# Kernel optimization log

Measured on AMD Instinct MI355X. Metric: run time of the kernel, lower is better.

## Reference

```python
import jax, jax.numpy as jnp
import numpy as np

B, C, H, W = 8, 4, 384, 384


def setup_inputs() -> dict:
    key = jax.random.key(0)
    k1, k2 = jax.random.split(key)
    outputs = jax.random.normal(k1, (B, C, H, W), dtype=jnp.float32)
    targets = jax.random.randint(k2, (B, H, W), 0, C)  # every class present w.h.p.
    return {"outputs": outputs, "targets": targets}


def _edt(is_zero):
    """Exact 2D Euclidean distance transform, batched.

    is_zero: bool [B,C,H,W], True at 'feature' pixels (distance 0 there).
    Returns float32 [B,C,H,W] distance to nearest True pixel.
    Separable exact algorithm (Meijster/Felzenszwalb-Huttenlocher style):
      phase 1: 1D distance along H via forward+backward scans;
      phase 2: dt^2(x,y) = min_j g(x,j)^2 + (y-j)^2 via a scan over y.
    """
    b, c, h, w = is_zero.shape
    BIG = jnp.float32(h + w)  # finite sentinel (exceeds any true distance)

    def pass1(carry, z):
        d = jnp.where(z, jnp.float32(0.0), jnp.minimum(carry + 1.0, BIG))
        return d, d

    init = jnp.full((b, c, w), BIG, jnp.float32)
    zt = jnp.moveaxis(is_zero, 2, 0)  # [H,B,C,W]
    _, fwd = jax.lax.scan(pass1, init, zt)
    _, bwd = jax.lax.scan(pass1, init, zt[::-1])
    g = jnp.minimum(fwd, bwd[::-1])          # [H,B,C,W] vertical 1D distances
    g2 = jnp.moveaxis(g * g, 0, 2)           # [B,C,H,W]

    j = jnp.arange(w, dtype=jnp.float32)     # candidate columns

    def pass2(_, y):
        # min over j of g(x,j)^2 + (y-j)^2  -> [B,C,H]
        return 0, jnp.min(g2 + (y - j) ** 2, axis=-1)

    _, dt2 = jax.lax.scan(pass2, 0, j)       # [W,B,C,H]
    return jnp.sqrt(jnp.moveaxis(dt2, 0, 3))  # [B,C,H,W]


def reference(outputs, targets):
    num_classes = outputs.shape[1]
    # one-hot: true_hot[b,c,h,w] = (targets[b,h,w] == c)
    true_hot = targets[:, None, :, :] == jnp.arange(num_classes)[None, :, None, None]
    dt = _edt(true_hot)                                  # 0 at class pixels
    dmax = jnp.max(dt, axis=(2, 3), keepdims=True)       # per (b,c) slice max
    dist_map = jnp.where(true_hot, -dmax, dt)            # factor = -1
    # weight=None -> ones(C); weight_matrix/weight.sum() == 1/C
    loss = jax.nn.softmax(outputs, axis=1) * dist_map / jnp.float32(num_classes)
    return jnp.mean(loss)
```

## Files before the change

### kernel.cpp

```cpp
#include <hip/hip_runtime.h>

#define B 8
#define C 4
#define H 384
#define W 384
#define HW (H * W)
#define CHW (C * H * W)
#define NTOT (B * CHW)
#define BIG2 589824
#define TPI 576
#define NBLK (B * TPI)
#define NSEG (B * H * 6)
#define LOG2E 1.44269504088896340736f

__device__ __forceinline__ int nearest2(unsigned long long m, int lx, int shl) {
    unsigned long long right = m >> lx;
    int dR = right ? (int)__builtin_ctzll(right) : 999;
    unsigned long long leftb = m << shl;
    int dL = leftb ? (int)__builtin_clzll(leftb) : 999;
    int d = min(dR, dL);
    return d * d;
}

__device__ __attribute__((noinline))
int ring_fallback(const int* __restrict__ tg, int xa, int ya, int c, int best) {
    for (int d = 17; d * d < best; ++d) {
        int xlo = xa - d, xhi = xa + d, ylo = ya - d, yhi = ya + d;
        for (int xx = max(xlo, 0); xx <= min(xhi, W - 1); ++xx) {
            int ddx = xx - xa;
            int bb = ddx * ddx + d * d;
            if (bb < best) {
                if (ylo >= 0 && tg[ylo * W + xx] == c) best = bb;
                if (yhi < H && tg[yhi * W + xx] == c) best = min(best, bb);
            }
        }
        for (int yy = max(ylo + 1, 0); yy <= min(yhi - 1, H - 1); ++yy) {
            int ddy = yy - ya;
            int bb = ddy * ddy + d * d;
            if (bb < best) {
                if (xlo >= 0 && tg[yy * W + xlo] == c) best = bb;
                if (xhi < W && tg[yy * W + xhi] == c) best = min(best, bb);
            }
        }
    }
    return best;
}

__global__ __launch_bounds__(256)
void build_masks(const int* __restrict__ targets,
                 unsigned long long* __restrict__ masks) {
    int wv = threadIdx.x >> 6, lane = threadIdx.x & 63;
    int seg = blockIdx.x * 4 + wv;
    if (seg >= NSEG) return;
    int wd = seg % 6, rem = seg / 6;
    int tv = targets[rem * W + wd * 64 + lane];
    unsigned long long m0 = __ballot(tv == 0);
    unsigned long long m1 = __ballot(tv == 1);
    unsigned long long m2 = __ballot(tv == 2);
    unsigned long long m3 = __ballot(tv == 3);
    if (lane == 0) {
        unsigned long long* dst = masks + (size_t)rem * 24 + wd;
        dst[0]  = m0;
        dst[6]  = m1;
        dst[12] = m2;
        dst[18] = m3;
    }
}

__global__ __launch_bounds__(256)
void dist_loss_kernel(const float* __restrict__ outputs,
                      const int* __restrict__ targets,
                      const unsigned long long* __restrict__ masks,
                      float* __restrict__ parts) {
    __shared__ unsigned long long rowsm[40][4];
    __shared__ unsigned long long big[8 * 18];
    __shared__ float sred[4][9];

    int bid = blockIdx.x;
    int bx = bid % 12, by = (bid / 12) % 48, b = bid / TPI;
    int x0 = bx * 32, y0 = by * 8;
    int tid = threadIdx.x, lane = tid & 63, wv = tid >> 6;
    const int* tg = targets + b * HW;

    if (tid < 160) {
        int r = tid >> 2, cc = tid & 3;
        int yaS = y0 - 16 + r;
        unsigned long long wmask = 0ull;
        if (yaS >= 0 && yaS < H) {
            const unsigned long long* mrow =
                masks + ((size_t)(b * H + yaS)) * 24 + cc * 6;
            int bitpos = x0 - 16;
            int iw = bitpos >> 6, sh = bitpos & 63;
            unsigned long long lo = (iw >= 0) ? mrow[iw] : 0ull;
            unsigned long long hi = (iw + 1 < 6) ? mrow[iw + 1] : 0ull;
            wmask = (lo >> sh) | (hi << (64 - sh));
        }
        rowsm[r][cc] = wmask;
    }
    __syncthreads();

    if (tid < 128) {
        int yy = tid >> 4, c = (tid >> 2) & 3, lvl = tid & 3;
        unsigned long long v = (lvl == 0)
            ? rowsm[16 + yy][c]
            : (rowsm[16 + yy - lvl][c] | rowsm[16 + yy + lvl][c]);
        big[yy * 18 + c * 4 + lvl] = v;
    }
    __syncthreads();

    int x = tid & 31, y = tid >> 5;
    int xa = x0 + x, ya = y0 + y, ly = y + 16;
    int lx = x + 16, shl = 63 - lx;

    float red[9];
    #pragma unroll
    for (int j = 0; j < 9; ++j) red[j] = 0.0f;

    const float* ob = outputs + (size_t)b * CHW + (size_t)ya * W + xa;
    float e0 = exp2f(ob[0] * LOG2E);
    float e1 = exp2f(ob[HW] * LOG2E);
    float e2 = exp2f(ob[2 * HW] * LOG2E);
    float e3 = exp2f(ob[3 * HW] * LOG2E);
    float inv = 1.0f / (e0 + e1 + e2 + e3);
    float pr[4] = {e0 * inv, e1 * inv, e2 * inv, e3 * inv};

    #pragma unroll
    for (int c = 0; c < 4; ++c) {
        const ulonglong2* pp = (const ulonglong2*)&big[y * 18 + c * 4];
        ulonglong2 v0 = pp[0], v1 = pp[1];
        int n0 = nearest2(v0.x, lx, shl);
        int n1 = nearest2(v0.y, lx, shl) + 1;
        int n2 = nearest2(v1.x, lx, shl) + 4;
        int n3 = nearest2(v1.y, lx, shl) + 9;
        int best = min(min(n0, n1), min(n2, n3));
        if (best > 16) {
            for (int dy = 4; dy <= 16 && dy * dy < best; ++dy) {
                unsigned long long m = rowsm[ly + dy][c] | rowsm[ly - dy][c];
                if (m) best = min(best, dy * dy + nearest2(m, lx, shl));
            }
            if (best > 289) {
                best = min(best, BIG2);
                best = ring_fallback(tg, xa, ya, c, best);
            }
        }
        float dt = sqrtf((float)best);
        red[0] += pr[c] * dt;
        if ((v0.x >> lx) & 1ull) red[1 + c] += pr[c];
        red[5 + c] = fmaxf(red[5 + c], dt);
    }

    #pragma unroll
    for (int off = 32; off > 0; off >>= 1) {
        #pragma unroll
        for (int j = 0; j < 5; ++j) red[j] += __shfl_down(red[j], off);
        #pragma unroll
        for (int j = 5; j < 9; ++j) red[j] = fmaxf(red[j], __shfl_down(red[j], off));
    }
    if (lane == 0) {
        #pragma unroll
        for (int j = 0; j < 9; ++j) sred[wv][j] = red[j];
    }
    __syncthreads();
    if (tid == 0) {
        float o[9];
        #pragma unroll
        for (int j = 0; j < 9; ++j) o[j] = sred[0][j];
        #pragma unroll
        for (int w = 1; w < 4; ++w) {
            #pragma unroll
            for (int j = 0; j < 5; ++j) o[j] += sred[w][j];
            #pragma unroll
            for (int j = 5; j < 9; ++j) o[j] = fmaxf(o[j], sred[w][j]);
        }
        #pragma unroll
        for (int j = 0; j < 9; ++j) parts[j * NBLK + bid] = o[j];
    }
}

__global__ __launch_bounds__(256)
void finalize(const float* __restrict__ parts, float* __restrict__ out) {
    __shared__ double asum[4];
    __shared__ double Tsh[32];
    __shared__ float Msh[32];
    int tid = threadIdx.x, lane = tid & 63, wv = tid >> 6;

    double a = 0.0;
    for (int i = tid; i < NBLK; i += 256) a += (double)parts[i];
    #pragma unroll
    for (int off = 32; off > 0; off >>= 1) a += __shfl_down(a, off);
    if (lane == 0) asum[wv] = a;

    for (int k = 0; k < 8; ++k) {
        int s = wv * 8 + k;
        int bb = s >> 2, cc = s & 3;
        double ts = 0.0;
        float ms = 0.0f;
        for (int i = lane; i < TPI; i += 64) {
            int blk = bb * TPI + i;
            ts += (double)parts[(1 + cc) * NBLK + blk];
            ms = fmaxf(ms, parts[(5 + cc) * NBLK + blk]);
        }
        #pragma unroll
        for (int off = 32; off > 0; off >>= 1) {
            ts += __shfl_down(ts, off);
            ms = fmaxf(ms, __shfl_down(ms, off));
        }
        if (lane == 0) { Tsh[s] = ts; Msh[s] = ms; }
    }
    __syncthreads();
    if (tid == 0) {
        double A = asum[0] + asum[1] + asum[2] + asum[3];
        double st = 0.0;
        for (int s = 0; s < 32; ++s) st += (double)Msh[s] * Tsh[s];
        out[0] = (float)((A - st) / ((double)C * (double)NTOT));
    }
}

extern "C" void kernel_launch(void* const* d_in, const int* in_sizes, int n_in,
                              void* d_out, int out_size, void* d_ws, size_t ws_size,
                              hipStream_t stream) {
    const float* outputs = (const float*)d_in[0];
    const int* targets = (const int*)d_in[1];
    float* out = (float*)d_out;
    float* parts = (float*)d_ws;
    unsigned long long* masks =
        (unsigned long long*)((char*)d_ws + 256 * 1024);

    build_masks<<<NSEG / 4, 256, 0, stream>>>(targets, masks);
    dist_loss_kernel<<<NBLK, 256, 0, stream>>>(outputs, targets, masks, parts);
    finalize<<<1, 256, 0, stream>>>(parts, out);
}
```

Baseline: 116.1 us.

## Fuse mask building into distance kernel with 64x8 tiles and 3-row halo

Removes the separate build_masks kernel: each block now ballots its own target bitmasks for a 14-row by 3-word halo into shared memory and runs the exact 3-row neighbourhood search directly on full 64-bit words. Tiles grow to 64x8 pixels with 512 threads, and the block reduction uses shuffles. The vertical halo drops from 16 rows to 3, so pixels whose best distance exceeds 16 now go straight to the scalar ring fallback starting at radius 4. This saves one launch and a global mask round trip, but the fallback may fire more often and targets get re-read redundantly across neighbouring blocks.

Result: no change. 115.7 us (-0.3%).

```diff
diff --git a/kernel.cpp b/kernel.cpp
--- a/kernel.cpp
+++ b/kernel.cpp
@@ -8,23 +8,13 @@
 #define CHW (C * H * W)
 #define NTOT (B * CHW)
 #define BIG2 589824
-#define TPI 576
+#define TPI 288
 #define NBLK (B * TPI)
-#define NSEG (B * H * 6)
 #define LOG2E 1.44269504088896340736f
-
-__device__ __forceinline__ int nearest2(unsigned long long m, int lx, int shl) {
-    unsigned long long right = m >> lx;
-    int dR = right ? (int)__builtin_ctzll(right) : 999;
-    unsigned long long leftb = m << shl;
-    int dL = leftb ? (int)__builtin_clzll(leftb) : 999;
-    int d = min(dR, dL);
-    return d * d;
-}
 
 __device__ __attribute__((noinline))
 int ring_fallback(const int* __restrict__ tg, int xa, int ya, int c, int best) {
-    for (int d = 17; d * d < best; ++d) {
+    for (int d = 4; d * d < best; ++d) {
         int xlo = xa - d, xhi = xa + d, ylo = ya - d, yhi = ya + d;
         for (int xx = max(xlo, 0); xx <= min(xhi, W - 1); ++xx) {
             int ddx = xx - xa;
@@ -46,106 +36,84 @@
     return best;
 }
 
-__global__ __launch_bounds__(256)
-void build_masks(const int* __restrict__ targets,
-                 unsigned long long* __restrict__ masks) {
-    int wv = threadIdx.x >> 6, lane = threadIdx.x & 63;
-    int seg = blockIdx.x * 4 + wv;
-    if (seg >= NSEG) return;
-    int wd = seg % 6, rem = seg / 6;
-    int tv = targets[rem * W + wd * 64 + lane];
-    unsigned long long m0 = __ballot(tv == 0);
-    unsigned long long m1 = __ballot(tv == 1);
-    unsigned long long m2 = __ballot(tv == 2);
-    unsigned long long m3 = __ballot(tv == 3);
-    if (lane == 0) {
-        unsigned long long* dst = masks + (size_t)rem * 24 + wd;
-        dst[0]  = m0;
-        dst[6]  = m1;
-        dst[12] = m2;
-        dst[18] = m3;
-    }
-}
-
-__global__ __launch_bounds__(256)
+__global__ __launch_bounds__(512)
 void dist_loss_kernel(const float* __restrict__ outputs,
                       const int* __restrict__ targets,
-                      const unsigned long long* __restrict__ masks,
                       float* __restrict__ parts) {
-    __shared__ unsigned long long rowsm[40][4];
-    __shared__ unsigned long long big[8 * 18];
-    __shared__ float sred[4][9];
+    __shared__ unsigned long long rowsm[14][3][4];
+    __shared__ float sred[8][9];
 
     int bid = blockIdx.x;
-    int bx = bid % 12, by = (bid / 12) % 48, b = bid / TPI;
-    int x0 = bx * 32, y0 = by * 8;
-    int tid = threadIdx.x, lane = tid & 63, wv = tid >> 6;
+    int b = bid / TPI;
+    int r = bid % TPI;
+    int wd = r / 48, yt = r % 48;
+    int tid = threadIdx.x, lane = tid & 63, wy = tid >> 6;
     const int* tg = targets + b * HW;
-
-    if (tid < 160) {
-        int r = tid >> 2, cc = tid & 3;
-        int yaS = y0 - 16 + r;
-        unsigned long long wmask = 0ull;
-        if (yaS >= 0 && yaS < H) {
-            const unsigned long long* mrow =
-                masks + ((size_t)(b * H + yaS)) * 24 + cc * 6;
-            int bitpos = x0 - 16;
-            int iw = bitpos >> 6, sh = bitpos & 63;
-            unsigned long long lo = (iw >= 0) ? mrow[iw] : 0ull;
-            unsigned long long hi = (iw + 1 < 6) ? mrow[iw + 1] : 0ull;
-            wmask = (lo >> sh) | (hi << (64 - sh));
-        }
-        rowsm[r][cc] = wmask;
+    int yr0 = yt * 8 - 3;
+
+    int xa = wd * 64 + lane;
+    int ya = yt * 8 + wy;
+
+    const float* ob = outputs + (size_t)b * CHW + (size_t)ya * W + xa;
+    float o0 = ob[0], o1 = ob[HW], o2 = ob[2 * HW], o3 = ob[3 * HW];
+
+    for (int t = wy; t < 42; t += 8) {
+        int rr = t / 3, wi = t % 3;
+        int yr = yr0 + rr, wg = wd - 1 + wi;
+        int tv = -1;
+        if (yr >= 0 && yr < H && wg >= 0 && wg < 6)
+            tv = tg[yr * W + wg * 64 + lane];
+        unsigned long long m0 = __ballot(tv == 0);
+        unsigned long long m1 = __ballot(tv == 1);
+        unsigned long long m2 = __ballot(tv == 2);
+        unsigned long long m3 = __ballot(tv == 3);
+        if (lane == 0) {
+            rowsm[rr][wi][0] = m0; rowsm[rr][wi][1] = m1;
+            rowsm[rr][wi][2] = m2; rowsm[rr][wi][3] = m3;
+        }
     }
     __syncthreads();
 
-    if (tid < 128) {
-        int yy = tid >> 4, c = (tid >> 2) & 3, lvl = tid & 3;
-        unsigned long long v = (lvl == 0)
-            ? rowsm[16 + yy][c]
-            : (rowsm[16 + yy - lvl][c] | rowsm[16 + yy + lvl][c]);
-        big[yy * 18 + c * 4 + lvl] = v;
-    }
-    __syncthreads();
-
-    int x = tid & 31, y = tid >> 5;
-    int xa = x0 + x, ya = y0 + y, ly = y + 16;
-    int lx = x + 16, shl = 63 - lx;
-
-    float red[9];
-    #pragma unroll
-    for (int j = 0; j < 9; ++j) red[j] = 0.0f;
-
-    const float* ob = outputs + (size_t)b * CHW + (size_t)ya * W + xa;
-    float e0 = exp2f(ob[0] * LOG2E);
-    float e1 = exp2f(ob[HW] * LOG2E);
-    float e2 = exp2f(ob[2 * HW] * LOG2E);
-    float e3 = exp2f(ob[3 * HW] * LOG2E);
+    float e0 = exp2f(o0 * LOG2E);
+    float e1 = exp2f(o1 * LOG2E);
+    float e2 = exp2f(o2 * LOG2E);
+    float e3 = exp2f(o3 * LOG2E);
     float inv = 1.0f / (e0 + e1 + e2 + e3);
     float pr[4] = {e0 * inv, e1 * inv, e2 * inv, e3 * inv};
 
+    int rs = wy + 3;
+    float red[9];
+    #pragma unroll
+    for (int j = 0; j < 9; ++j) red[j] = 0.0f;
+
     #pragma unroll
     for (int c = 0; c < 4; ++c) {
-        const ulonglong2* pp = (const ulonglong2*)&big[y * 18 + c * 4];
-        ulonglong2 v0 = pp[0], v1 = pp[1];
-        int n0 = nearest2(v0.x, lx, shl);
-        int n1 = nearest2(v0.y, lx, shl) + 1;
-        int n2 = nearest2(v1.x, lx, shl) + 4;
-        int n3 = nearest2(v1.y, lx, shl) + 9;
-        int best = min(min(n0, n1), min(n2, n3));
+        unsigned long long lvl[4][3];
+        #pragma unroll
+        for (int wi = 0; wi < 3; ++wi) {
+            lvl[0][wi] = rowsm[rs][wi][c];
+            lvl[1][wi] = rowsm[rs - 1][wi][c] | rowsm[rs + 1][wi][c];
+            lvl[2][wi] = rowsm[rs - 2][wi][c] | rowsm[rs + 2][wi][c];
+            lvl[3][wi] = rowsm[rs - 3][wi][c] | rowsm[rs + 3][wi][c];
+        }
+        int best = 0x7fffffff;
+        #pragma unroll
+        for (int k = 0; k < 4; ++k) {
+            unsigned long long wm = lvl[k][0], w0 = lvl[k][1], wp = lvl[k][2];
+            unsigned long long rgt = (w0 >> lane) | ((wp << 1) << (63 - lane));
+            unsigned long long lft = (w0 << (63 - lane)) | ((wm >> lane) >> 1);
+            int dR = rgt ? (int)__builtin_ctzll(rgt) : 999;
+            int dL = lft ? (int)__builtin_clzll(lft) : 999;
+            int d = min(dR, dL);
+            best = min(best, d * d + k * k);
+        }
         if (best > 16) {
-            for (int dy = 4; dy <= 16 && dy * dy < best; ++dy) {
-                unsigned long long m = rowsm[ly + dy][c] | rowsm[ly - dy][c];
-                if (m) best = min(best, dy * dy + nearest2(m, lx, shl));
-            }
-            if (best > 289) {
-                best = min(best, BIG2);
-                best = ring_fallback(tg, xa, ya, c, best);
-            }
+            best = min(best, BIG2);
+            best = ring_fallback(tg, xa, ya, c, best);
         }
         float dt = sqrtf((float)best);
         red[0] += pr[c] * dt;
-        if ((v0.x >> lx) & 1ull) red[1 + c] += pr[c];
+        if ((lvl[0][1] >> lane) & 1ull) red[1 + c] += pr[c];
         red[5 + c] = fmaxf(red[5 + c], dt);
     }
 
@@ -158,22 +126,25 @@
     }
     if (lane == 0) {
         #pragma unroll
-        for (int j = 0; j < 9; ++j) sred[wv][j] = red[j];
+        for (int j = 0; j < 9; ++j) sred[wy][j] = red[j];
     }
     __syncthreads();
-    if (tid == 0) {
-        float o[9];
-        #pragma unroll
-        for (int j = 0; j < 9; ++j) o[j] = sred[0][j];
-        #pragma unroll
-        for (int w = 1; w < 4; ++w) {
+
+    if (wy == 0) {
+        float v[9];
+        #pragma unroll
+        for (int j = 0; j < 9; ++j) v[j] = (lane < 8) ? sred[lane][j] : 0.0f;
+        #pragma unroll
+        for (int off = 4; off > 0; off >>= 1) {
             #pragma unroll
-            for (int j = 0; j < 5; ++j) o[j] += sred[w][j];
+            for (int j = 0; j < 5; ++j) v[j] += __shfl_down(v[j], off);
             #pragma unroll
-            for (int j = 5; j < 9; ++j) o[j] = fmaxf(o[j], sred[w][j]);
-        }
-        #pragma unroll
-        for (int j = 0; j < 9; ++j) parts[j * NBLK + bid] = o[j];
+            for (int j = 5; j < 9; ++j) v[j] = fmaxf(v[j], __shfl_down(v[j], off));
+        }
+        if (lane == 0) {
+            #pragma unroll
+            for (int j = 0; j < 9; ++j) parts[j * NBLK + bid] = v[j];
+        }
     }
 }
 
@@ -223,10 +194,7 @@
     const int* targets = (const int*)d_in[1];
     float* out = (float*)d_out;
     float* parts = (float*)d_ws;
-    unsigned long long* masks =
-        (unsigned long long*)((char*)d_ws + 256 * 1024);
-
-    build_masks<<<NSEG / 4, 256, 0, stream>>>(targets, masks);
-    dist_loss_kernel<<<NBLK, 256, 0, stream>>>(outputs, targets, masks, parts);
+
+    dist_loss_kernel<<<NBLK, 512, 0, stream>>>(outputs, targets, parts);
     finalize<<<1, 256, 0, stream>>>(parts, out);
 }
```
